# Kernel tuning notes

Measured on AMD Instinct MI355X. Metric: run time of the kernel, lower is better.

Reference implementation:

```python
import jax, jax.numpy as jnp
import numpy as np

N = 524288   # total nodes
B = 16384    # num graphs
D = 64       # node feature dim
STEPS = 2    # set2set processing steps


def _lin_params(key, out_dim, in_dim):
    k1, k2 = jax.random.split(key)
    s = 1.0 / np.sqrt(in_dim)
    W = jax.random.uniform(k1, (out_dim, in_dim), jnp.float32, -s, s)
    b = jax.random.uniform(k2, (out_dim,), jnp.float32, -s, s)
    return W, b


def setup_inputs() -> dict:
    key = jax.random.key(0)
    ks = jax.random.split(key, 16)
    inp = {}
    inp["features"] = jax.random.normal(ks[0], (N, D), jnp.float32)
    inp["batch_index"] = jnp.sort(jax.random.randint(ks[1], (N,), 0, B, dtype=jnp.int64))
    inp["eps_gate"] = jax.random.uniform(ks[2], (N, 1), jnp.float32)
    inp["noise"] = jax.random.uniform(ks[3], (N, D), jnp.float32)
    # compressor: Linear(64,64) -> BatchNorm1d(64) -> ReLU -> Linear(64,1)
    inp["c_w1"], inp["c_b1"] = _lin_params(ks[4], D, D)
    inp["bn_g"] = jnp.ones((D,), jnp.float32)
    inp["bn_b"] = jnp.zeros((D,), jnp.float32)
    inp["c_w2"], inp["c_b2"] = _lin_params(ks[5], 1, D)
    # set2set LSTM: input 2D, hidden D (gate order i,f,g,o)
    s = 1.0 / np.sqrt(D)
    inp["lstm_wih"] = jax.random.uniform(ks[6], (4 * D, 2 * D), jnp.float32, -s, s)
    inp["lstm_whh"] = jax.random.uniform(ks[7], (4 * D, D), jnp.float32, -s, s)
    inp["lstm_bih"] = jax.random.uniform(ks[8], (4 * D,), jnp.float32, -s, s)
    inp["lstm_bhh"] = jax.random.uniform(ks[9], (4 * D,), jnp.float32, -s, s)
    # predictor: 128->256->128->64
    inp["p_w1"], inp["p_b1"] = _lin_params(ks[10], 256, 2 * D)
    inp["p_w2"], inp["p_b2"] = _lin_params(ks[11], 128, 256)
    inp["p_w3"], inp["p_b3"] = _lin_params(ks[12], 64, 128)
    return inp


def _forward(features, batch_index, eps_gate, noise,
             c_w1, c_b1, bn_g, bn_b, c_w2, c_b2,
             lstm_wih, lstm_whh, lstm_bih, lstm_bhh,
             p_w1, p_b1, p_w2, p_b2, p_w3, p_b3):
    idx = batch_index
    seg_sum = lambda v: jax.ops.segment_sum(v, idx, num_segments=B)

    # ---- compressor (BatchNorm in training mode: batch stats, biased var) ----
    h = features @ c_w1.T + c_b1                       # [N, D]
    mu = h.mean(axis=0)
    var = ((h - mu) ** 2).mean(axis=0)
    h = (h - mu) * jax.lax.rsqrt(var + 1e-5) * bn_g + bn_b
    h = jax.nn.relu(h)
    p = h @ c_w2.T + c_b2                              # [N, 1]

    # ---- concrete gate ----
    bias = 1e-4
    eps = (bias - (1.0 - bias)) * eps_gate + (1.0 - bias)   # uniform in (bias, 1-bias)
    gate_inputs = jnp.log(eps) - jnp.log(1.0 - eps)
    lambda_pos = jax.nn.sigmoid(gate_inputs + p)       # [N, 1] (temperature = 1)
    lambda_neg = 1.0 - lambda_pos
    preserve_rate = (jax.nn.sigmoid(p) > 0.5).astype(jnp.float32).mean()

    # ---- per-graph mean / unbiased std of detached features ----
    static = jax.lax.stop_gradient(features)
    counts = seg_sum(jnp.ones((N,), jnp.float32))       # [B]
    mean_g = seg_sum(static) / jnp.maximum(counts, 1.0)[:, None]   # [B, D]
    diff = static - mean_g[idx]
    var_g = seg_sum(diff * diff) / jnp.maximum(counts - 1.0, 1.0)[:, None]
    std_g = jnp.sqrt(var_g)                             # [B, D]
    node_mean = mean_g[idx]                             # [N, D]
    node_std = std_g[idx]                               # [N, D]

    # ---- noisy reparameterization ----
    noisy_mean = lambda_pos * features + lambda_neg * node_mean
    noisy_std = lambda_neg * node_std
    noisy = noisy_mean + noise * noisy_std              # [N, D]

    # ---- Set2Set readout ----
    q_star = jnp.zeros((B, 2 * D), jnp.float32)
    hh = jnp.zeros((B, D), jnp.float32)
    cc = jnp.zeros((B, D), jnp.float32)
    for _ in range(STEPS):
        gates = q_star @ lstm_wih.T + hh @ lstm_whh.T + lstm_bih + lstm_bhh
        i, f, g, o = jnp.split(gates, 4, axis=-1)
        cc = jax.nn.sigmoid(f) * cc + jax.nn.sigmoid(i) * jnp.tanh(g)
        hh = jax.nn.sigmoid(o) * jnp.tanh(cc)
        q = hh                                          # [B, D]
        e = jnp.sum(noisy * q[idx], axis=-1)            # [N]
        m = jax.ops.segment_max(e, idx, num_segments=B)
        w = jnp.exp(e - m[idx])
        denom = seg_sum(w)
        a = w / denom[idx]                              # segment softmax
        r = seg_sum(a[:, None] * noisy)                 # [B, D]
        q_star = jnp.concatenate([q, r], axis=-1)

    # ---- KL ----
    epsl = 1e-7
    t1 = 0.5 * seg_sum(jnp.mean(noisy_std ** 2 / (node_std + epsl) ** 2, axis=1))[:, None]
    t2 = seg_sum(((noisy_mean - node_mean) / (node_std + epsl)) ** 2)
    KL_Loss = jnp.mean(t1 + t2)

    # ---- predictor ----
    z = jax.nn.relu(q_star @ p_w1.T + p_b1)
    z = jax.nn.relu(z @ p_w2.T + p_b2)
    predictions = z @ p_w3.T + p_b3                     # [B, 64]
    return predictions, KL_Loss, preserve_rate, lambda_pos


def reference(features, batch_index, eps_gate, noise,
              c_w1, c_b1, bn_g, bn_b, c_w2, c_b2,
              lstm_wih, lstm_whh, lstm_bih, lstm_bhh,
              p_w1, p_b1, p_w2, p_b2, p_w3, p_b3):
    return _forward(features, batch_index, eps_gate, noise,
                    c_w1, c_b1, bn_g, bn_b, c_w2, c_b2,
                    lstm_wih, lstm_whh, lstm_bih, lstm_bhh,
                    p_w1, p_b1, p_w2, p_b2, p_w3, p_b3)
```

## Files before the change

### kernel.cpp

```cpp
#include <hip/hip_runtime.h>
#include <math.h>

#define N_TOT 524288
#define B_GR  16384
#define CAPR  64

#define LOG2E 1.44269504088896f
#define LN2   0.69314718055995f

typedef __attribute__((ext_vector_type(8))) short bf16x8;
typedef __attribute__((ext_vector_type(4))) float f32x4;

__device__ __forceinline__ float fexp2(float x) { return __builtin_amdgcn_exp2f(x); }
__device__ __forceinline__ float flog2(float x) { return __builtin_amdgcn_logf(x); }
__device__ __forceinline__ float frcp(float x)  { return __builtin_amdgcn_rcpf(x); }
__device__ __forceinline__ float sigf(float x)  { return frcp(1.0f + fexp2(-x * LOG2E)); }

__device__ __forceinline__ unsigned int f2bf(float x) {
  unsigned int u = __float_as_uint(x);
  return (u + 0x7FFFu + ((u >> 16) & 1u)) >> 16;
}
__device__ __forceinline__ float bf2f(unsigned int s) {
  return __uint_as_float(s << 16);
}

template <int CTRL>
__device__ __forceinline__ float dppadd(float v) {
  return v + __int_as_float(__builtin_amdgcn_update_dpp(
      0, __float_as_int(v), CTRL, 0xF, 0xF, true));
}
__device__ __forceinline__ float wave_red(float v) {
  v = dppadd<0x111>(v);
  v = dppadd<0x112>(v);
  v = dppadd<0x114>(v);
  v = dppadd<0x118>(v);
  v = dppadd<0x142>(v);
  v = dppadd<0x143>(v);
  return __int_as_float(__builtin_amdgcn_readlane(__float_as_int(v), 63));
}

__device__ __forceinline__ void load_A64(const float* __restrict__ A, size_t lda, int n0, int k0,
                                         float (*As)[68], int tid) {
#pragma unroll
  for (int s = 0; s < 4; s++) {
    int e4 = tid * 4 + s * 1024;
    int r = e4 >> 6, k = e4 & 63;
    *(float4*)&As[r][k] = *(const float4*)&A[(size_t)(n0 + r) * lda + k0 + k];
  }
}
__device__ __forceinline__ void mm64(const float (*As)[68], const float (*Wt)[68],
                                     int ty, int tx, float acc[4][4]) {
#pragma unroll
  for (int k4 = 0; k4 < 64; k4 += 4) {
    float4 b0 = *(const float4*)&Wt[k4 + 0][tx * 4];
    float4 b1 = *(const float4*)&Wt[k4 + 1][tx * 4];
    float4 b2 = *(const float4*)&Wt[k4 + 2][tx * 4];
    float4 b3 = *(const float4*)&Wt[k4 + 3][tx * 4];
#pragma unroll
    for (int i = 0; i < 4; i++) {
      float4 a = *(const float4*)&As[ty * 4 + i][k4];
      acc[i][0] = fmaf(a.w, b3.x, fmaf(a.z, b2.x, fmaf(a.y, b1.x, fmaf(a.x, b0.x, acc[i][0]))));
      acc[i][1] = fmaf(a.w, b3.y, fmaf(a.z, b2.y, fmaf(a.y, b1.y, fmaf(a.x, b0.y, acc[i][1]))));
      acc[i][2] = fmaf(a.w, b3.z, fmaf(a.z, b2.z, fmaf(a.y, b1.z, fmaf(a.x, b0.z, acc[i][2]))));
      acc[i][3] = fmaf(a.w, b3.w, fmaf(a.z, b2.w, fmaf(a.y, b1.w, fmaf(a.x, b0.w, acc[i][3]))));
    }
  }
}

__global__ void k_offsets(const int* __restrict__ idx, int* __restrict__ off) {
  int b = blockIdx.x * blockDim.x + threadIdx.x;
  if (b > B_GR) return;
  if (b == B_GR) { off[B_GR] = N_TOT; return; }
  int lo = 0, hi = N_TOT;
  while (lo < hi) { int mid = (lo + hi) >> 1; if (idx[mid] < b) lo = mid + 1; else hi = mid; }
  off[b] = lo;
}

__global__ void k_prep(const float* __restrict__ w1, const float* __restrict__ pw1,
                       const float* __restrict__ pw2, const float* __restrict__ pw3,
                       const float* __restrict__ wih,
                       float* __restrict__ pw1T, float* __restrict__ pw2T,
                       float* __restrict__ pw3T, float* __restrict__ rtg,
                       unsigned short* __restrict__ wfragb) {
  int t = blockIdx.x * 256 + threadIdx.x;
  for (int i = t; i < 256 * 128; i += 16384){ int r = i >> 7, c = i & 127; pw1T[c * 256 + r] = pw1[i]; }
  for (int i = t; i < 128 * 256; i += 16384){ int r = i >> 8, c = i & 255; pw2T[c * 128 + r] = pw2[i]; }
  for (int i = t; i < 64 * 128; i += 16384) { int r = i >> 7, c = i & 127; pw3T[c * 64 + r]  = pw3[i]; }
  for (int i = t; i < 64 * 64 * 4; i += 16384) {
    int k = i >> 8, rem = i & 255, d = rem >> 2, j = rem & 3;
    rtg[i] = wih[(size_t)(j * 64 + d) * 128 + 64 + k];
  }
  for (int i = t; i < 8 * 64 * 8; i += 16384) {
    int f = i >> 9, lane = (i >> 3) & 63, j = i & 7;
    int ct = f >> 1, kh = f & 1;
    int k = kh * 32 + (lane >> 4) * 8 + j;
    int col = ct * 16 + (lane & 15);
    wfragb[i] = (unsigned short)f2bf(w1[(size_t)col * 64 + k]);
  }
}

__global__ __launch_bounds__(256) void k_bn_stats(const float* __restrict__ X,
                                                  const unsigned short* __restrict__ wfragb,
                                                  const float* __restrict__ b1, unsigned short* __restrict__ h,
                                                  float* __restrict__ pSum, float* __restrict__ pSq) {
  __shared__ float redS[16][64];
  __shared__ float redQ[16][64];
  int tid = threadIdx.x, w = tid >> 6, l = tid & 63;
  int n0 = blockIdx.x * 64;
  int r0 = w * 16;
  int arow = n0 + r0 + (l & 15);
  int kb = (l >> 4) * 8;
  const float* xr = X + (size_t)arow * 64 + kb;
  float4 a00 = *(const float4*)&xr[0];
  float4 a01 = *(const float4*)&xr[4];
  float4 a10 = *(const float4*)&xr[32];
  float4 a11 = *(const float4*)&xr[36];
  bf16x8 A0, A1;
  A0[0] = (short)f2bf(a00.x); A0[1] = (short)f2bf(a00.y); A0[2] = (short)f2bf(a00.z); A0[3] = (short)f2bf(a00.w);
  A0[4] = (short)f2bf(a01.x); A0[5] = (short)f2bf(a01.y); A0[6] = (short)f2bf(a01.z); A0[7] = (short)f2bf(a01.w);
  A1[0] = (short)f2bf(a10.x); A1[1] = (short)f2bf(a10.y); A1[2] = (short)f2bf(a10.z); A1[3] = (short)f2bf(a10.w);
  A1[4] = (short)f2bf(a11.x); A1[5] = (short)f2bf(a11.y); A1[6] = (short)f2bf(a11.z); A1[7] = (short)f2bf(a11.w);
  const bf16x8* wf = (const bf16x8*)wfragb;
  f32x4 acc0 = {0.f, 0.f, 0.f, 0.f}, acc1 = acc0, acc2 = acc0, acc3 = acc0;
  {
    bf16x8 B00 = wf[0 * 64 + l], B01 = wf[1 * 64 + l];
    bf16x8 B10 = wf[2 * 64 + l], B11 = wf[3 * 64 + l];
    bf16x8 B20 = wf[4 * 64 + l], B21 = wf[5 * 64 + l];
    bf16x8 B30 = wf[6 * 64 + l], B31 = wf[7 * 64 + l];
    acc0 = __builtin_amdgcn_mfma_f32_16x16x32_bf16(A0, B00, acc0, 0, 0, 0);
    acc0 = __builtin_amdgcn_mfma_f32_16x16x32_bf16(A1, B01, acc0, 0, 0, 0);
    acc1 = __builtin_amdgcn_mfma_f32_16x16x32_bf16(A0, B10, acc1, 0, 0, 0);
    acc1 = __builtin_amdgcn_mfma_f32_16x16x32_bf16(A1, B11, acc1, 0, 0, 0);
    acc2 = __builtin_amdgcn_mfma_f32_16x16x32_bf16(A0, B20, acc2, 0, 0, 0);
    acc2 = __builtin_amdgcn_mfma_f32_16x16x32_bf16(A1, B21, acc2, 0, 0, 0);
    acc3 = __builtin_amdgcn_mfma_f32_16x16x32_bf16(A0, B30, acc3, 0, 0, 0);
    acc3 = __builtin_amdgcn_mfma_f32_16x16x32_bf16(A1, B31, acc3, 0, 0, 0);
  }
  int c16 = l & 15, rgrp = l >> 4;
  int slot = w * 4 + rgrp;
#pragma unroll
  for (int ct = 0; ct < 4; ct++) {
    f32x4 acc = (ct == 0) ? acc0 : (ct == 1) ? acc1 : (ct == 2) ? acc2 : acc3;
    int col = ct * 16 + c16;
    float bb = b1[col];
    float cs = 0.f, cq = 0.f;
#pragma unroll
    for (int j = 0; j < 4; j++) {
      float hv = acc[j] + bb;
      int row = n0 + r0 + rgrp * 4 + j;
      h[(size_t)row * 64 + col] = (unsigned short)f2bf(hv);
      cs += hv; cq = fmaf(hv, hv, cq);
    }
    redS[slot][col] = cs;
    redQ[slot][col] = cq;
  }
  __syncthreads();
  if (tid < 64) {
    float s = 0.f, q = 0.f;
#pragma unroll
    for (int t = 0; t < 16; t++) { s += redS[t][tid]; q += redQ[t][tid]; }
    pSum[(size_t)blockIdx.x * 64 + tid] = s;
    pSq[(size_t)blockIdx.x * 64 + tid] = q;
  }
}

__global__ __launch_bounds__(256) void k_bn_final(const float* __restrict__ pSum, const float* __restrict__ pSq,
                                                  const float* __restrict__ bn_g, const float* __restrict__ bn_b,
                                                  float* __restrict__ aff) {
  int c = blockIdx.x;
  float s = 0, q = 0;
  for (int i = threadIdx.x; i < 8192; i += 256) {
    s += pSum[(size_t)i * 64 + c];
    q += pSq[(size_t)i * 64 + c];
  }
  __shared__ float rs[256], rq[256];
  rs[threadIdx.x] = s; rq[threadIdx.x] = q;
  __syncthreads();
  for (int st = 128; st > 0; st >>= 1) {
    if (threadIdx.x < st) { rs[threadIdx.x] += rs[threadIdx.x + st]; rq[threadIdx.x] += rq[threadIdx.x + st]; }
    __syncthreads();
  }
  if (threadIdx.x == 0) {
    float mu = rs[0] / (float)N_TOT;
    float var = rq[0] / (float)N_TOT - mu * mu;
    var = fmaxf(var, 0.0f);
    float A = bn_g[c] * rsqrtf(var + 1e-5f);
    aff[c] = A;
    aff[64 + c] = bn_b[c] - mu * A;
  }
}

__global__ __launch_bounds__(256) void k_lstm1(const float* __restrict__ bih, const float* __restrict__ bhh,
                                               const float* __restrict__ wih, const float* __restrict__ whh,
                                               float* __restrict__ q1, float* __restrict__ c1, float* __restrict__ sh2) {
  __shared__ float g1[256];
  __shared__ float q1s[64];
  int tid = threadIdx.x;
  g1[tid] = bih[tid] + bhh[tid];
  __syncthreads();
  if (tid < 64) {
    float ig = sigf(g1[tid]);
    float gg = tanhf(g1[128 + tid]);
    float cc = ig * gg;
    float og = sigf(g1[192 + tid]);
    float qv = og * tanhf(cc);
    q1s[tid] = qv; q1[tid] = qv; c1[tid] = cc;
  }
  __syncthreads();
  float acc = g1[tid];
  for (int k = 0; k < 64; k++)
    acc = fmaf(wih[(size_t)tid * 128 + k] + whh[(size_t)tid * 64 + k], q1s[k], acc);
  sh2[tid] = acc;
}

__global__ __launch_bounds__(256) void k_gate_h(const unsigned short* __restrict__ h, const float* __restrict__ aff,
                                                const float* __restrict__ w2, const float* __restrict__ cb2,
                                                const float* __restrict__ eps_gate,
                                                float* __restrict__ lamWS, float* __restrict__ lamOut,
                                                int* __restrict__ presPart) {
  __shared__ float Hs[64][65];
  __shared__ float A2s[64], C2s[64], w2s[64];
  __shared__ int pcnt[4];
  int tid = threadIdx.x;
  if (tid < 64) { A2s[tid] = aff[tid]; C2s[tid] = aff[64 + tid]; w2s[tid] = w2[tid]; }
  int n0 = blockIdx.x * 64;
#pragma unroll
  for (int s = 0; s < 4; s++) {
    int e4 = tid * 4 + s * 1024;
    int r = e4 >> 6, c = e4 & 63;
    ushort4 v = *(const ushort4*)&h[(size_t)(n0 + r) * 64 + c];
    Hs[r][c] = bf2f(v.x); Hs[r][c + 1] = bf2f(v.y);
    Hs[r][c + 2] = bf2f(v.z); Hs[r][c + 3] = bf2f(v.w);
  }
  __syncthreads();
  int r = tid >> 2, q = tid & 3;
  float p = 0.f;
#pragma unroll
  for (int j = 0; j < 16; j++) {
    int d = q * 16 + j;
    p = fmaf(fmaxf(fmaf(Hs[r][d], A2s[d], C2s[d]), 0.f), w2s[d], p);
  }
  p += __shfl_xor(p, 1);
  p += __shfl_xor(p, 2);
  p += cb2[0];
  unsigned long long m = __ballot(q == 0 && p > 0.0f);
  if ((tid & 63) == 0) pcnt[tid >> 6] = (int)__popcll(m);
  if (q == 0) {
    int row = n0 + r;
    float eg = eps_gate[row];
    float eps = 0.9999f - 0.9998f * eg;
    float gi = (flog2(eps) - flog2(1.0f - eps)) * LN2;
    float lam = sigf(gi + p);
    lamWS[row] = lam;
    lamOut[row] = lam;
  }
  __syncthreads();
  if (tid == 0) presPart[blockIdx.x] = pcnt[0] + pcnt[1] + pcnt[2] + pcnt[3];
}

__global__ __launch_bounds__(256) void k_graph_reg(const float* __restrict__ X, const float* __restrict__ noise,
                                                   const float* __restrict__ lam, const int* __restrict__ off,
                                                   const float* __restrict__ q1g, const float* __restrict__ c1g,
                                                   const float* __restrict__ sh2g, const float* __restrict__ rtg,
                                                   unsigned short* __restrict__ noisyFB, float* __restrict__ qstar,
                                                   float* __restrict__ klp) {
  int wg = blockIdx.x * 4 + (threadIdx.x >> 6);
  int lane = threadIdx.x & 63;
  int n0 = off[wg], cnt = off[wg + 1] - n0;
  const float THR = 8.f;
  const float* xp = X + (size_t)n0 * 64 + lane;
  const float* zp = noise + (size_t)n0 * 64 + lane;
  float r1v = 0.f;
  bool fits = (cnt <= CAPR);
  unsigned int pk[CAPR / 2];

  if (cnt > 0 && fits) {
    float s0 = 0.f, q0 = 0.f, s1 = 0.f, q1_ = 0.f;
#pragma unroll
    for (int np = 0; np < CAPR / 2; np++) {
      int n = 2 * np;
      if (n < cnt) {
        float a = xp[(size_t)n * 64];
        s0 += a; q0 = fmaf(a, a, q0);
        float b = 0.f;
        if (n + 1 < cnt) {
          b = xp[(size_t)(n + 1) * 64];
          s1 += b; q1_ = fmaf(b, b, q1_);
        }
        pk[np] = (f2bf(b) << 16) | f2bf(a);
      }
    }
    float c = (float)cnt;
    float mean = (s0 + s1) / c;
    float var = fmaxf(((q0 + q1_) - c * mean * mean) / fmaxf(c - 1.f, 1.f), 0.f);
    float sd = sqrtf(var);
    float inv = frcp(sd + 1e-7f);
    float S1 = wave_red(sd * sd * inv * inv);
    float q1v2 = q1g[lane] * LOG2E;
    float t2acc = 0.f, sumOm2 = 0.f;
    float m0 = -INFINITY, l0 = 0.f, r0 = 0.f;
    float m1 = -INFINITY, l1 = 0.f, r1a = 0.f;
#pragma unroll
    for (int np = 0; np < CAPR / 2; np++) {
      int n = 2 * np;
      if (n < cnt) {
        bool hasB = (n + 1 < cnt);
        unsigned int p2 = pk[np];
        float xA = bf2f(p2 & 0xffffu), xB = bf2f(p2 >> 16);
        float lamA = lam[n0 + n];
        float zA = zp[(size_t)n * 64];
        float lamB = hasB ? lam[n0 + n + 1] : 0.f;
        float zB = hasB ? zp[(size_t)(n + 1) * 64] : 0.f;
        float omA = 1.f - lamA, omB = 1.f - lamB;
        float nvA = fmaf(lamA, xA, omA * mean) + zA * (omA * sd);
        float nvB = fmaf(lamB, xB, omB * mean) + zB * (omB * sd);
        pk[np] = (f2bf(nvB) << 16) | f2bf(nvA);
        float ldA = lamA * (xA - mean) * inv; t2acc = fmaf(ldA, ldA, t2acc);
        sumOm2 = fmaf(omA, omA, sumOm2);
        if (hasB) {
          float ldB = lamB * (xB - mean) * inv; t2acc = fmaf(ldB, ldB, t2acc);
          sumOm2 = fmaf(omB, omB, sumOm2);
        }
        float e0 = wave_red(nvA * q1v2);
        float e1 = hasB ? wave_red(nvB * q1v2) : 0.f;
        if (e0 > m0 + THR) { float sc = fexp2(m0 - e0); l0 *= sc; r0 *= sc; m0 = e0; }
        float pA = fexp2(e0 - m0); l0 += pA; r0 = fmaf(pA, nvA, r0);
        if (hasB) {
          if (e1 > m1 + THR) { float sc = fexp2(m1 - e1); l1 *= sc; r1a *= sc; m1 = e1; }
          float pB = fexp2(e1 - m1); l1 += pB; r1a = fmaf(pB, nvB, r1a);
        }
      }
    }
    float M = fmaxf(m0, m1);
    float sc0 = fexp2(m0 - M), sc1 = (m1 == -INFINITY) ? 0.f : fexp2(m1 - M);
    float L = l0 * sc0 + l1 * sc1;
    float R = r0 * sc0 + r1a * sc1;
    r1v = R / L;
    float t2tot = wave_red(t2acc);
    if (lane == 0) klp[wg] = fmaf(0.5f * sumOm2, S1, t2tot);
  } else if (cnt > 0) {
    unsigned short* nw = noisyFB + (size_t)n0 * 64 + lane;
    float s0 = 0.f, q0 = 0.f;
    for (int n = 0; n < cnt; n++) { float a = xp[(size_t)n * 64]; s0 += a; q0 = fmaf(a, a, q0); }
    float c = (float)cnt;
    float mean = s0 / c;
    float var = fmaxf((q0 - c * mean * mean) / fmaxf(c - 1.f, 1.f), 0.f);
    float sd = sqrtf(var);
    float inv = frcp(sd + 1e-7f);
    float S1 = wave_red(sd * sd * inv * inv);
    float q1v2 = q1g[lane] * LOG2E;
    float t2acc = 0.f, sumOm2 = 0.f;
    float m0 = -INFINITY, l0 = 0.f, r0 = 0.f;
    for (int n = 0; n < cnt; n++) {
      float lamA = lam[n0 + n];
      float xA = xp[(size_t)n * 64];
      float zA = zp[(size_t)n * 64];
      float omA = 1.f - lamA;
      float nvA = fmaf(lamA, xA, omA * mean) + zA * (omA * sd);
      nw[(size_t)n * 64] = (unsigned short)f2bf(nvA);
      float ldA = lamA * (xA - mean) * inv; t2acc = fmaf(ldA, ldA, t2acc);
      sumOm2 = fmaf(omA, omA, sumOm2);
      float e0 = wave_red(nvA * q1v2);
      if (e0 > m0 + THR) { float sc = fexp2(m0 - e0); l0 *= sc; r0 *= sc; m0 = e0; }
      float pA = fexp2(e0 - m0); l0 += pA; r0 = fmaf(pA, nvA, r0);
    }
    r1v = r0 / l0;
    float t2tot = wave_red(t2acc);
    if (lane == 0) klp[wg] = fmaf(0.5f * sumOm2, S1, t2tot);
  } else {
    if (lane == 0) klp[wg] = 0.0f;
  }

  float a0 = 0.f, a1 = 0.f, a2 = 0.f, a3 = 0.f;
  const float4* rt = (const float4*)rtg;
#pragma unroll 4
  for (int k = 0; k < 64; k++) {
    float rk = __shfl(r1v, k);
    float4 w = rt[k * 64 + lane];
    a0 = fmaf(w.x, rk, a0); a1 = fmaf(w.y, rk, a1);
    a2 = fmaf(w.z, rk, a2); a3 = fmaf(w.w, rk, a3);
  }
  float ig = a0 + sh2g[lane];
  float fg = a1 + sh2g[64 + lane];
  float gg = a2 + sh2g[128 + lane];
  float og = a3 + sh2g[192 + lane];
  float c2 = sigf(fg) * c1g[lane] + sigf(ig) * tanhf(gg);
  float q2 = sigf(og) * tanhf(c2);
  qstar[(size_t)wg * 128 + lane] = q2;

  float r2v = 0.f;
  if (cnt > 0) {
    float q2v2 = q2 * LOG2E;
    float m0 = -INFINITY, l0 = 0.f, r0 = 0.f;
    float m1 = -INFINITY, l1 = 0.f, r1a = 0.f;
    if (fits) {
#pragma unroll
      for (int np = 0; np < CAPR / 2; np++) {
        int n = 2 * np;
        if (n < cnt) {
          bool hasB = (n + 1 < cnt);
          unsigned int p2 = pk[np];
          float nvA = bf2f(p2 & 0xffffu), nvB = bf2f(p2 >> 16);
          float e0 = wave_red(nvA * q2v2);
          float e1 = hasB ? wave_red(nvB * q2v2) : 0.f;
          if (e0 > m0 + THR) { float sc = fexp2(m0 - e0); l0 *= sc; r0 *= sc; m0 = e0; }
          float pA = fexp2(e0 - m0); l0 += pA; r0 = fmaf(pA, nvA, r0);
          if (hasB) {
            if (e1 > m1 + THR) { float sc = fexp2(m1 - e1); l1 *= sc; r1a *= sc; m1 = e1; }
            float pB = fexp2(e1 - m1); l1 += pB; r1a = fmaf(pB, nvB, r1a);
          }
        }
      }
    } else {
      const unsigned short* np_ = noisyFB + (size_t)n0 * 64 + lane;
      for (int n = 0; n < cnt; n++) {
        float nvA = bf2f(np_[(size_t)n * 64]);
        float e0 = wave_red(nvA * q2v2);
        if (e0 > m0 + THR) { float sc = fexp2(m0 - e0); l0 *= sc; r0 *= sc; m0 = e0; }
        float pA = fexp2(e0 - m0); l0 += pA; r0 = fmaf(pA, nvA, r0);
      }
    }
    float M = fmaxf(m0, m1);
    float sc0 = fexp2(m0 - M), sc1 = (m1 == -INFINITY) ? 0.f : fexp2(m1 - M);
    float L = l0 * sc0 + l1 * sc1;
    float R = r0 * sc0 + r1a * sc1;
    r2v = R / L;
  }
  qstar[(size_t)wg * 128 + 64 + lane] = r2v;
}

template <int KDIM, int ODIM, bool RELU>
__global__ __launch_bounds__(256) void k_linear(const float* __restrict__ A, const float* __restrict__ WT,
                                                const float* __restrict__ bias, float* __restrict__ C) {
  __shared__ float As[64][68];
  __shared__ float Wt[64][68];
  int tid = threadIdx.x, ty = tid >> 4, tx = tid & 15;
  int n0 = blockIdx.x * 64, c0 = blockIdx.y * 64;
  float acc[4][4] = {};
  for (int kt = 0; kt < KDIM; kt += 64) {
    __syncthreads();
    load_A64(A, KDIM, n0, kt, As, tid);
    load_A64(WT, ODIM, kt, c0, Wt, tid);
    __syncthreads();
    mm64(As, Wt, ty, tx, acc);
  }
#pragma unroll
  for (int i = 0; i < 4; i++) {
    int row = n0 + ty * 4 + i;
    float4 o;
    float v0 = acc[i][0] + bias[c0 + tx * 4 + 0];
    float v1 = acc[i][1] + bias[c0 + tx * 4 + 1];
    float v2 = acc[i][2] + bias[c0 + tx * 4 + 2];
    float v3 = acc[i][3] + bias[c0 + tx * 4 + 3];
    if (RELU) { v0 = fmaxf(v0, 0.f); v1 = fmaxf(v1, 0.f); v2 = fmaxf(v2, 0.f); v3 = fmaxf(v3, 0.f); }
    o.x = v0; o.y = v1; o.z = v2; o.w = v3;
    *(float4*)&C[(size_t)row * ODIM + c0 + tx * 4] = o;
  }
}

__global__ __launch_bounds__(256) void k_final(const float* __restrict__ klp, const int* __restrict__ presPart,
                                               float* __restrict__ out) {
  __shared__ float red[256];
  __shared__ int redi[256];
  float s = 0.0f;
  int pc = 0;
  for (int i = threadIdx.x; i < B_GR; i += 256) s += klp[i];
  for (int i = threadIdx.x; i < 8192; i += 256) pc += presPart[i];
  red[threadIdx.x] = s;
  redi[threadIdx.x] = pc;
  __syncthreads();
  for (int st = 128; st > 0; st >>= 1) {
    if (threadIdx.x < st) {
      red[threadIdx.x] += red[threadIdx.x + st];
      redi[threadIdx.x] += redi[threadIdx.x + st];
    }
    __syncthreads();
  }
  if (threadIdx.x == 0) {
    out[(size_t)B_GR * 64] = red[0] / (float)(B_GR * 64);
    out[(size_t)B_GR * 64 + 1] = (float)redi[0] / (float)N_TOT;
  }
}

extern "C" void kernel_launch(void* const* d_in, const int* in_sizes, int n_in,
                              void* d_out, int out_size, void* d_ws, size_t ws_size,
                              hipStream_t stream) {
  const float* features = (const float*)d_in[0];
  const int*   bidx     = (const int*)d_in[1];
  const float* eps_gate = (const float*)d_in[2];
  const float* noise    = (const float*)d_in[3];
  const float* c_w1 = (const float*)d_in[4];
  const float* c_b1 = (const float*)d_in[5];
  const float* bn_g = (const float*)d_in[6];
  const float* bn_b = (const float*)d_in[7];
  const float* c_w2 = (const float*)d_in[8];
  const float* c_b2 = (const float*)d_in[9];
  const float* wih  = (const float*)d_in[10];
  const float* whh  = (const float*)d_in[11];
  const float* bih  = (const float*)d_in[12];
  const float* bhh  = (const float*)d_in[13];
  const float* p_w1 = (const float*)d_in[14];
  const float* p_b1 = (const float*)d_in[15];
  const float* p_w2 = (const float*)d_in[16];
  const float* p_b2 = (const float*)d_in[17];
  const float* p_w3 = (const float*)d_in[18];
  const float* p_b3 = (const float*)d_in[19];
  float* out = (float*)d_out;

  float* wsf   = (float*)d_ws;
  int*   offp  = (int*)wsf;
  float* pSum  = wsf + 16448;
  float* pSq   = pSum + 524288;
  float* aff   = pSq + 524288;
  float* q1w   = aff + 128;
  float* c1w   = q1w + 64;
  float* sh2w  = c1w + 64;
  float* lamw  = sh2w + 256;
  float* pw1T  = lamw + (size_t)N_TOT;
  float* pw2T  = pw1T + 32768;
  float* pw3T  = pw2T + 32768;
  float* rtgw  = pw3T + 8192;
  unsigned short* wfragb = (unsigned short*)(rtgw + 16384);
  float* hwf   = rtgw + 16384 + 2048;
  unsigned short* hb = (unsigned short*)hwf;
  unsigned short* noisyFB = hb;
  float* qstarw = hwf + (size_t)N_TOT * 64;
  float* z1w    = qstarw + (size_t)B_GR * 128;
  float* z2w    = z1w + (size_t)B_GR * 256;
  float* klpw   = z2w + (size_t)B_GR * 128;
  int*   presPart = (int*)(klpw + B_GR);

  float* lamOut = out + (size_t)B_GR * 64 + 2;

  k_offsets<<<(B_GR + 1 + 255) / 256, 256, 0, stream>>>(bidx, offp);
  k_prep<<<64, 256, 0, stream>>>(c_w1, p_w1, p_w2, p_w3, wih, pw1T, pw2T, pw3T, rtgw, wfragb);
  k_bn_stats<<<N_TOT / 64, 256, 0, stream>>>(features, wfragb, c_b1, hb, pSum, pSq);
  k_bn_final<<<64, 256, 0, stream>>>(pSum, pSq, bn_g, bn_b, aff);
  k_lstm1<<<1, 256, 0, stream>>>(bih, bhh, wih, whh, q1w, c1w, sh2w);
  k_gate_h<<<N_TOT / 64, 256, 0, stream>>>(hb, aff, c_w2, c_b2, eps_gate, lamw, lamOut, presPart);
  k_graph_reg<<<B_GR / 4, 256, 0, stream>>>(features, noise, lamw, offp, q1w, c1w, sh2w, rtgw,
                                            noisyFB, qstarw, klpw);
  k_linear<128, 256, true><<<dim3(B_GR / 64, 4), 256, 0, stream>>>(qstarw, pw1T, p_b1, z1w);
  k_linear<256, 128, true><<<dim3(B_GR / 64, 2), 256, 0, stream>>>(z1w, pw2T, p_b2, z2w);
  k_linear<128, 64, false><<<dim3(B_GR / 64, 1), 256, 0, stream>>>(z2w, pw3T, p_b3, out);
  k_final<<<1, 256, 0, stream>>>(klpw, presPart, out);
}
```

Before: 292.1 us.

## Batch segment attention dot products with butterfly transpose-reduction across lanes

Replaces the per-node serial wave reductions and online softmax in the set2set attention with a batched scheme. All 64 node-feature dot products are reduced at once via a recursive-halving merge (shuffle-xor transpose), so each lane ends up holding one node's score. A single max, exp and sum across the wave replace the online-softmax rescaling, and the readout loop broadcasts weights by shuffle. This removes the long chain of dependent DPP reductions per node at the cost of always processing all 64 slots, padding short segments with zeros.

```diff
diff --git a/kernel.cpp b/kernel.cpp
--- a/kernel.cpp
+++ b/kernel.cpp
@@ -37,6 +37,53 @@
   v = dppadd<0x142>(v);
   v = dppadd<0x143>(v);
   return __int_as_float(__builtin_amdgcn_readlane(__float_as_int(v), 63));
+}
+
+__device__ __forceinline__ float mergeRed(float a, float b, int off, int lane) {
+  float as = __shfl_xor(a, off);
+  float bs = __shfl_xor(b, off);
+  return (lane & off) ? (b + bs) : (a + as);
+}
+
+__device__ __forceinline__ float attn_batched(const unsigned int (&pk)[CAPR / 2], int cnt,
+                                              float qv2, int lane) {
+  float m2[16];
+#pragma unroll
+  for (int k = 0; k < 16; k++) {
+    unsigned int pa = pk[2 * k], pb = pk[2 * k + 1];
+    float a0 = bf2f(pa & 0xffffu) * qv2;
+    float a1 = bf2f(pa >> 16) * qv2;
+    float b0 = bf2f(pb & 0xffffu) * qv2;
+    float b1 = bf2f(pb >> 16) * qv2;
+    float u = mergeRed(a0, a1, 1, lane);
+    float v = mergeRed(b0, b1, 1, lane);
+    m2[k] = mergeRed(u, v, 2, lane);
+  }
+#pragma unroll
+  for (int k = 0; k < 8; k++) m2[k] = mergeRed(m2[2 * k], m2[2 * k + 1], 4, lane);
+#pragma unroll
+  for (int k = 0; k < 4; k++) m2[k] = mergeRed(m2[2 * k], m2[2 * k + 1], 8, lane);
+#pragma unroll
+  for (int k = 0; k < 2; k++) m2[k] = mergeRed(m2[2 * k], m2[2 * k + 1], 16, lane);
+  float e = mergeRed(m2[0], m2[1], 32, lane);
+  e = (lane < cnt) ? e : -3.0e38f;
+  float M = e;
+#pragma unroll
+  for (int off = 32; off > 0; off >>= 1) M = fmaxf(M, __shfl_xor(M, off));
+  float w = fexp2(e - M);
+  float denom = w;
+#pragma unroll
+  for (int off = 32; off > 0; off >>= 1) denom += __shfl_xor(denom, off);
+  float racc = 0.f;
+#pragma unroll
+  for (int np = 0; np < CAPR / 2; np++) {
+    unsigned int p2 = pk[np];
+    float wA = __shfl(w, 2 * np);
+    float wB = __shfl(w, 2 * np + 1);
+    racc = fmaf(wA, bf2f(p2 & 0xffffu), racc);
+    racc = fmaf(wB, bf2f(p2 >> 16), racc);
+  }
+  return racc / denom;
 }
 
 __device__ __forceinline__ void load_A64(const float* __restrict__ A, size_t lda, int n0, int k0,
@@ -288,6 +335,8 @@
           s1 += b; q1_ = fmaf(b, b, q1_);
         }
         pk[np] = (f2bf(b) << 16) | f2bf(a);
+      } else {
+        pk[np] = 0u;
       }
     }
     float c = (float)cnt;
@@ -296,10 +345,7 @@
     float sd = sqrtf(var);
     float inv = frcp(sd + 1e-7f);
     float S1 = wave_red(sd * sd * inv * inv);
-    float q1v2 = q1g[lane] * LOG2E;
     float t2acc = 0.f, sumOm2 = 0.f;
-    float m0 = -INFINITY, l0 = 0.f, r0 = 0.f;
-    float m1 = -INFINITY, l1 = 0.f, r1a = 0.f;
 #pragma unroll
     for (int np = 0; np < CAPR / 2; np++) {
       int n = 2 * np;
@@ -314,28 +360,16 @@
         float omA = 1.f - lamA, omB = 1.f - lamB;
         float nvA = fmaf(lamA, xA, omA * mean) + zA * (omA * sd);
         float nvB = fmaf(lamB, xB, omB * mean) + zB * (omB * sd);
-        pk[np] = (f2bf(nvB) << 16) | f2bf(nvA);
+        pk[np] = hasB ? ((f2bf(nvB) << 16) | f2bf(nvA)) : f2bf(nvA);
         float ldA = lamA * (xA - mean) * inv; t2acc = fmaf(ldA, ldA, t2acc);
         sumOm2 = fmaf(omA, omA, sumOm2);
         if (hasB) {
           float ldB = lamB * (xB - mean) * inv; t2acc = fmaf(ldB, ldB, t2acc);
           sumOm2 = fmaf(omB, omB, sumOm2);
         }
-        float e0 = wave_red(nvA * q1v2);
-        float e1 = hasB ? wave_red(nvB * q1v2) : 0.f;
-        if (e0 > m0 + THR) { float sc = fexp2(m0 - e0); l0 *= sc; r0 *= sc; m0 = e0; }
-        float pA = fexp2(e0 - m0); l0 += pA; r0 = fmaf(pA, nvA, r0);
-        if (hasB) {
-          if (e1 > m1 + THR) { float sc = fexp2(m1 - e1); l1 *= sc; r1a *= sc; m1 = e1; }
-          float pB = fexp2(e1 - m1); l1 += pB; r1a = fmaf(pB, nvB, r1a);
-        }
       }
     }
-    float M = fmaxf(m0, m1);
-    float sc0 = fexp2(m0 - M), sc1 = (m1 == -INFINITY) ? 0.f : fexp2(m1 - M);
-    float L = l0 * sc0 + l1 * sc1;
-    float R = r0 * sc0 + r1a * sc1;
-    r1v = R / L;
+    r1v = attn_batched(pk, cnt, q1g[lane] * LOG2E, lane);
     float t2tot = wave_red(t2acc);
     if (lane == 0) klp[wg] = fmaf(0.5f * sumOm2, S1, t2tot);
   } else if (cnt > 0) {
@@ -391,40 +425,20 @@
   float r2v = 0.f;
   if (cnt > 0) {
     float q2v2 = q2 * LOG2E;
-    float m0 = -INFINITY, l0 = 0.f, r0 = 0.f;
-    float m1 = -INFINITY, l1 = 0.f, r1a = 0.f;
     if (fits) {
-#pragma unroll
-      for (int np = 0; np < CAPR / 2; np++) {
-        int n = 2 * np;
-        if (n < cnt) {
-          bool hasB = (n + 1 < cnt);
-          unsigned int p2 = pk[np];
-          float nvA = bf2f(p2 & 0xffffu), nvB = bf2f(p2 >> 16);
-          float e0 = wave_red(nvA * q2v2);
-          float e1 = hasB ? wave_red(nvB * q2v2) : 0.f;
-          if (e0 > m0 + THR) { float sc = fexp2(m0 - e0); l0 *= sc; r0 *= sc; m0 = e0; }
-          float pA = fexp2(e0 - m0); l0 += pA; r0 = fmaf(pA, nvA, r0);
-          if (hasB) {
-            if (e1 > m1 + THR) { float sc = fexp2(m1 - e1); l1 *= sc; r1a *= sc; m1 = e1; }
-            float pB = fexp2(e1 - m1); l1 += pB; r1a = fmaf(pB, nvB, r1a);
-          }
-        }
-      }
+      r2v = attn_batched(pk, cnt, q2v2, lane);
     } else {
+      const float THR2 = 8.f;
       const unsigned short* np_ = noisyFB + (size_t)n0 * 64 + lane;
+      float m0 = -INFINITY, l0 = 0.f, r0 = 0.f;
       for (int n = 0; n < cnt; n++) {
         float nvA = bf2f(np_[(size_t)n * 64]);
         float e0 = wave_red(nvA * q2v2);
-        if (e0 > m0 + THR) { float sc = fexp2(m0 - e0); l0 *= sc; r0 *= sc; m0 = e0; }
+        if (e0 > m0 + THR2) { float sc = fexp2(m0 - e0); l0 *= sc; r0 *= sc; m0 = e0; }
         float pA = fexp2(e0 - m0); l0 += pA; r0 = fmaf(pA, nvA, r0);
       }
-    }
-    float M = fmaxf(m0, m1);
-    float sc0 = fexp2(m0 - M), sc1 = (m1 == -INFINITY) ? 0.f : fexp2(m1 - M);
-    float L = l0 * sc0 + l1 * sc1;
-    float R = r0 * sc0 + r1a * sc1;
-    r2v = R / L;
+      r2v = r0 / l0;
+    }
   }
   qstar[(size_t)wg * 128 + 64 + lane] = r2v;
 }
```

After: 368.0 us. +26.0%, slower.

## Run predictor MLP on bf16 MFMA with pre-swizzled weight fragments

Applied to the files above, without the earlier changes.

The three predictor linear layers move from an fp32 LDS-tiled FMA GEMM to bf16 MFMA 16x16x32 instructions. Weights are pre-packed into fragment layout in k_prep, and the q_star, z1 and z2 intermediates are stored as bf16, which halves their memory traffic. This cuts the FMA-bound GEMM cost at the price of bf16 rounding in activations and weights, which could affect accuracy tolerance.

```diff
diff --git a/kernel.cpp b/kernel.cpp
--- a/kernel.cpp
+++ b/kernel.cpp
@@ -39,34 +39,6 @@
   return __int_as_float(__builtin_amdgcn_readlane(__float_as_int(v), 63));
 }
 
-__device__ __forceinline__ void load_A64(const float* __restrict__ A, size_t lda, int n0, int k0,
-                                         float (*As)[68], int tid) {
-#pragma unroll
-  for (int s = 0; s < 4; s++) {
-    int e4 = tid * 4 + s * 1024;
-    int r = e4 >> 6, k = e4 & 63;
-    *(float4*)&As[r][k] = *(const float4*)&A[(size_t)(n0 + r) * lda + k0 + k];
-  }
-}
-__device__ __forceinline__ void mm64(const float (*As)[68], const float (*Wt)[68],
-                                     int ty, int tx, float acc[4][4]) {
-#pragma unroll
-  for (int k4 = 0; k4 < 64; k4 += 4) {
-    float4 b0 = *(const float4*)&Wt[k4 + 0][tx * 4];
-    float4 b1 = *(const float4*)&Wt[k4 + 1][tx * 4];
-    float4 b2 = *(const float4*)&Wt[k4 + 2][tx * 4];
-    float4 b3 = *(const float4*)&Wt[k4 + 3][tx * 4];
-#pragma unroll
-    for (int i = 0; i < 4; i++) {
-      float4 a = *(const float4*)&As[ty * 4 + i][k4];
-      acc[i][0] = fmaf(a.w, b3.x, fmaf(a.z, b2.x, fmaf(a.y, b1.x, fmaf(a.x, b0.x, acc[i][0]))));
-      acc[i][1] = fmaf(a.w, b3.y, fmaf(a.z, b2.y, fmaf(a.y, b1.y, fmaf(a.x, b0.y, acc[i][1]))));
-      acc[i][2] = fmaf(a.w, b3.z, fmaf(a.z, b2.z, fmaf(a.y, b1.z, fmaf(a.x, b0.z, acc[i][2]))));
-      acc[i][3] = fmaf(a.w, b3.w, fmaf(a.z, b2.w, fmaf(a.y, b1.w, fmaf(a.x, b0.w, acc[i][3]))));
-    }
-  }
-}
-
 __global__ void k_offsets(const int* __restrict__ idx, int* __restrict__ off) {
   int b = blockIdx.x * blockDim.x + threadIdx.x;
   if (b > B_GR) return;
@@ -79,23 +51,41 @@
 __global__ void k_prep(const float* __restrict__ w1, const float* __restrict__ pw1,
                        const float* __restrict__ pw2, const float* __restrict__ pw3,
                        const float* __restrict__ wih,
-                       float* __restrict__ pw1T, float* __restrict__ pw2T,
-                       float* __restrict__ pw3T, float* __restrict__ rtg,
-                       unsigned short* __restrict__ wfragb) {
+                       float* __restrict__ rtg, unsigned short* __restrict__ wfragb,
+                       unsigned short* __restrict__ wf1, unsigned short* __restrict__ wf2,
+                       unsigned short* __restrict__ wf3) {
   int t = blockIdx.x * 256 + threadIdx.x;
-  for (int i = t; i < 256 * 128; i += 16384){ int r = i >> 7, c = i & 127; pw1T[c * 256 + r] = pw1[i]; }
-  for (int i = t; i < 128 * 256; i += 16384){ int r = i >> 8, c = i & 255; pw2T[c * 128 + r] = pw2[i]; }
-  for (int i = t; i < 64 * 128; i += 16384) { int r = i >> 7, c = i & 127; pw3T[c * 64 + r]  = pw3[i]; }
   for (int i = t; i < 64 * 64 * 4; i += 16384) {
     int k = i >> 8, rem = i & 255, d = rem >> 2, j = rem & 3;
     rtg[i] = wih[(size_t)(j * 64 + d) * 128 + 64 + k];
   }
   for (int i = t; i < 8 * 64 * 8; i += 16384) {
     int f = i >> 9, lane = (i >> 3) & 63, j = i & 7;
-    int ct = f >> 1, kh = f & 1;
-    int k = kh * 32 + (lane >> 4) * 8 + j;
+    int ct = f >> 1, kt = f & 1;
+    int k = kt * 32 + (lane >> 4) * 8 + j;
     int col = ct * 16 + (lane & 15);
     wfragb[i] = (unsigned short)f2bf(w1[(size_t)col * 64 + k]);
+  }
+  for (int i = t; i < 64 * 64 * 8; i += 16384) {
+    int f = i >> 9, lane = (i >> 3) & 63, j = i & 7;
+    int ct = f >> 2, kt = f & 3;
+    int k = kt * 32 + (lane >> 4) * 8 + j;
+    int col = ct * 16 + (lane & 15);
+    wf1[i] = (unsigned short)f2bf(pw1[(size_t)col * 128 + k]);
+  }
+  for (int i = t; i < 64 * 64 * 8; i += 16384) {
+    int f = i >> 9, lane = (i >> 3) & 63, j = i & 7;
+    int ct = f >> 3, kt = f & 7;
+    int k = kt * 32 + (lane >> 4) * 8 + j;
+    int col = ct * 16 + (lane & 15);
+    wf2[i] = (unsigned short)f2bf(pw2[(size_t)col * 256 + k]);
+  }
+  for (int i = t; i < 16 * 64 * 8; i += 16384) {
+    int f = i >> 9, lane = (i >> 3) & 63, j = i & 7;
+    int ct = f >> 2, kt = f & 3;
+    int k = kt * 32 + (lane >> 4) * 8 + j;
+    int col = ct * 16 + (lane & 15);
+    wf3[i] = (unsigned short)f2bf(pw3[(size_t)col * 128 + k]);
   }
 }
 
@@ -262,7 +252,7 @@
                                                    const float* __restrict__ lam, const int* __restrict__ off,
                                                    const float* __restrict__ q1g, const float* __restrict__ c1g,
                                                    const float* __restrict__ sh2g, const float* __restrict__ rtg,
-                                                   unsigned short* __restrict__ noisyFB, float* __restrict__ qstar,
+                                                   unsigned short* __restrict__ noisyFB, unsigned short* __restrict__ qstarb,
                                                    float* __restrict__ klp) {
   int wg = blockIdx.x * 4 + (threadIdx.x >> 6);
   int lane = threadIdx.x & 63;
@@ -386,7 +376,7 @@
   float og = a3 + sh2g[192 + lane];
   float c2 = sigf(fg) * c1g[lane] + sigf(ig) * tanhf(gg);
   float q2 = sigf(og) * tanhf(c2);
-  qstar[(size_t)wg * 128 + lane] = q2;
+  qstarb[(size_t)wg * 128 + lane] = (unsigned short)f2bf(q2);
 
   float r2v = 0.f;
   if (cnt > 0) {
@@ -426,35 +416,41 @@
     float R = r0 * sc0 + r1a * sc1;
     r2v = R / L;
   }
-  qstar[(size_t)wg * 128 + 64 + lane] = r2v;
-}
-
-template <int KDIM, int ODIM, bool RELU>
-__global__ __launch_bounds__(256) void k_linear(const float* __restrict__ A, const float* __restrict__ WT,
-                                                const float* __restrict__ bias, float* __restrict__ C) {
-  __shared__ float As[64][68];
-  __shared__ float Wt[64][68];
-  int tid = threadIdx.x, ty = tid >> 4, tx = tid & 15;
-  int n0 = blockIdx.x * 64, c0 = blockIdx.y * 64;
-  float acc[4][4] = {};
-  for (int kt = 0; kt < KDIM; kt += 64) {
-    __syncthreads();
-    load_A64(A, KDIM, n0, kt, As, tid);
-    load_A64(WT, ODIM, kt, c0, Wt, tid);
-    __syncthreads();
-    mm64(As, Wt, ty, tx, acc);
-  }
-#pragma unroll
-  for (int i = 0; i < 4; i++) {
-    int row = n0 + ty * 4 + i;
-    float4 o;
-    float v0 = acc[i][0] + bias[c0 + tx * 4 + 0];
-    float v1 = acc[i][1] + bias[c0 + tx * 4 + 1];
-    float v2 = acc[i][2] + bias[c0 + tx * 4 + 2];
-    float v3 = acc[i][3] + bias[c0 + tx * 4 + 3];
-    if (RELU) { v0 = fmaxf(v0, 0.f); v1 = fmaxf(v1, 0.f); v2 = fmaxf(v2, 0.f); v3 = fmaxf(v3, 0.f); }
-    o.x = v0; o.y = v1; o.z = v2; o.w = v3;
-    *(float4*)&C[(size_t)row * ODIM + c0 + tx * 4] = o;
+  qstarb[(size_t)wg * 128 + 64 + lane] = (unsigned short)f2bf(r2v);
+}
+
+template <int KDIM, int ODIM, bool RELU, bool OUTF32>
+__global__ __launch_bounds__(256) void k_linmfma(const unsigned short* __restrict__ A,
+                                                 const unsigned short* __restrict__ WF,
+                                                 const float* __restrict__ bias, void* __restrict__ Cv) {
+  constexpr int NKF = KDIM / 32;
+  constexpr int NCT = ODIM / 16;
+  int tid = threadIdx.x, w = tid >> 6, l = tid & 63;
+  int r0 = blockIdx.x * 64 + w * 16;
+  int arow = r0 + (l & 15);
+  int kb = (l >> 4) * 8;
+  bf16x8 Af[NKF];
+#pragma unroll
+  for (int kf = 0; kf < NKF; kf++)
+    Af[kf] = *(const bf16x8*)&A[(size_t)arow * KDIM + kf * 32 + kb];
+  const bf16x8* wf = (const bf16x8*)WF;
+  int c16 = l & 15, rg = l >> 4;
+#pragma unroll
+  for (int ct = 0; ct < NCT; ct++) {
+    f32x4 acc = {0.f, 0.f, 0.f, 0.f};
+#pragma unroll
+    for (int kf = 0; kf < NKF; kf++)
+      acc = __builtin_amdgcn_mfma_f32_16x16x32_bf16(Af[kf], wf[(ct * NKF + kf) * 64 + l], acc, 0, 0, 0);
+    int col = ct * 16 + c16;
+    float bb = bias[col];
+#pragma unroll
+    for (int j = 0; j < 4; j++) {
+      float v = acc[j] + bb;
+      if (RELU) v = fmaxf(v, 0.f);
+      int row = r0 + rg * 4 + j;
+      if (OUTF32) ((float*)Cv)[(size_t)row * ODIM + col] = v;
+      else ((unsigned short*)Cv)[(size_t)row * ODIM + col] = (unsigned short)f2bf(v);
+    }
   }
 }
 
@@ -516,32 +512,32 @@
   float* c1w   = q1w + 64;
   float* sh2w  = c1w + 64;
   float* lamw  = sh2w + 256;
-  float* pw1T  = lamw + (size_t)N_TOT;
-  float* pw2T  = pw1T + 32768;
-  float* pw3T  = pw2T + 32768;
-  float* rtgw  = pw3T + 8192;
+  float* rtgw  = lamw + (size_t)N_TOT;
   unsigned short* wfragb = (unsigned short*)(rtgw + 16384);
-  float* hwf   = rtgw + 16384 + 2048;
+  unsigned short* wf1 = wfragb + 4096;
+  unsigned short* wf2 = wf1 + 32768;
+  unsigned short* wf3 = wf2 + 32768;
+  float* hwf = (float*)(wf3 + 8192);
   unsigned short* hb = (unsigned short*)hwf;
   unsigned short* noisyFB = hb;
-  float* qstarw = hwf + (size_t)N_TOT * 64;
-  float* z1w    = qstarw + (size_t)B_GR * 128;
-  float* z2w    = z1w + (size_t)B_GR * 256;
-  float* klpw   = z2w + (size_t)B_GR * 128;
-  int*   presPart = (int*)(klpw + B_GR);
+  unsigned short* qstarb = (unsigned short*)(hwf + (size_t)N_TOT * 64);
+  unsigned short* z1b = qstarb + (size_t)B_GR * 128;
+  unsigned short* z2b = z1b + (size_t)B_GR * 256;
+  float* klpw = (float*)(z2b + (size_t)B_GR * 128);
+  int* presPart = (int*)(klpw + B_GR);
 
   float* lamOut = out + (size_t)B_GR * 64 + 2;
 
   k_offsets<<<(B_GR + 1 + 255) / 256, 256, 0, stream>>>(bidx, offp);
-  k_prep<<<64, 256, 0, stream>>>(c_w1, p_w1, p_w2, p_w3, wih, pw1T, pw2T, pw3T, rtgw, wfragb);
+  k_prep<<<64, 256, 0, stream>>>(c_w1, p_w1, p_w2, p_w3, wih, rtgw, wfragb, wf1, wf2, wf3);
   k_bn_stats<<<N_TOT / 64, 256, 0, stream>>>(features, wfragb, c_b1, hb, pSum, pSq);
   k_bn_final<<<64, 256, 0, stream>>>(pSum, pSq, bn_g, bn_b, aff);
   k_lstm1<<<1, 256, 0, stream>>>(bih, bhh, wih, whh, q1w, c1w, sh2w);
   k_gate_h<<<N_TOT / 64, 256, 0, stream>>>(hb, aff, c_w2, c_b2, eps_gate, lamw, lamOut, presPart);
   k_graph_reg<<<B_GR / 4, 256, 0, stream>>>(features, noise, lamw, offp, q1w, c1w, sh2w, rtgw,
-                                            noisyFB, qstarw, klpw);
-  k_linear<128, 256, true><<<dim3(B_GR / 64, 4), 256, 0, stream>>>(qstarw, pw1T, p_b1, z1w);
-  k_linear<256, 128, true><<<dim3(B_GR / 64, 2), 256, 0, stream>>>(z1w, pw2T, p_b2, z2w);
-  k_linear<128, 64, false><<<dim3(B_GR / 64, 1), 256, 0, stream>>>(z2w, pw3T, p_b3, out);
+                                            noisyFB, qstarb, klpw);
+  k_linmfma<128, 256, true, false><<<B_GR / 64, 256, 0, stream>>>(qstarb, wf1, p_b1, z1b);
+  k_linmfma<256, 128, true, false><<<B_GR / 64, 256, 0, stream>>>(z1b, wf2, p_b2, z2b);
+  k_linmfma<128, 64, false, true><<<B_GR / 64, 256, 0, stream>>>(z2b, wf3, p_b3, out);
   k_final<<<1, 256, 0, stream>>>(klpw, presPart, out);
 }
```

New measurement: 260.8 us. 10.7% less time.
